# Kernel tuning notes

Hardware: AMD Instinct MI355X
Metric: run time of the kernel (lower is better)

Reference implementation:

```python
import jax, jax.numpy as jnp
import numpy as np

L, M, K, H, F, D = 8, 32768, 8, 128, 32, 3  # fronts, nodes/front, in-degree, hidden, feat, depth-branches


def _resnet(x, w1, b1, w2, b2, w3, b3):
    # resnet module: lay3(tanh(lay2(tanh(lay1(x)))) + x)
    h1 = jnp.tanh(x @ w1 + b1)
    h2 = jnp.tanh(h1 @ w2 + b2)
    return (h2 + x) @ w3 + b3


def setup_inputs() -> dict:
    key = jax.random.key(0)
    ks = iter(jax.random.split(key, 80))

    def nrm(shape, fan_in):
        return jax.random.normal(next(ks), shape, jnp.float32) / np.float32(np.sqrt(fan_in))

    def bias(shape):
        return 0.01 * jax.random.normal(next(ks), shape, jnp.float32)

    inp = {}
    inp["node_feats"] = jax.random.normal(next(ks), (L, M, F), jnp.float32)
    inp["pred_idx"] = jax.random.randint(next(ks), (L - 1, M, K), 0, M, jnp.int32)
    inp["embed_w"] = nrm((F, H), F); inp["embed_b"] = bias((H,))
    # d{1,2,3}_mp_bwd and d{1,2,3}_mp_bwd1 : per-depth pair of H-resnets, stacked [D,2,...]
    inp["mp_w1"] = nrm((D, 2, H, H), H); inp["mp_b1"] = bias((D, 2, H))
    inp["mp_w2"] = nrm((D, 2, H, H), H); inp["mp_b2"] = bias((D, 2, H))
    inp["mp_w3"] = nrm((D, 2, H, H), H); inp["mp_b3"] = bias((D, 2, H))
    for p in ("comb", "node"):  # d*_comb_embed(+1), d*_node_embeds(+1)
        inp[p + "_wide_w1"] = nrm((D, 2 * H, 2 * H), 2 * H); inp[p + "_wide_b1"] = bias((D, 2 * H))
        inp[p + "_wide_w2"] = nrm((D, 2 * H, 2 * H), 2 * H); inp[p + "_wide_b2"] = bias((D, 2 * H))
        inp[p + "_wide_w3"] = nrm((D, 2 * H, H), 2 * H);     inp[p + "_wide_b3"] = bias((D, H))
        inp[p + "_h_w1"] = nrm((D, H, H), H); inp[p + "_h_b1"] = bias((D, H))
        inp[p + "_h_w2"] = nrm((D, H, H), H); inp[p + "_h_b2"] = bias((D, H))
        inp[p + "_h_w3"] = nrm((D, H, H), H); inp[p + "_h_b3"] = bias((D, H))
    return inp


def reference(node_feats, pred_idx, embed_w, embed_b,
              mp_w1, mp_b1, mp_w2, mp_b2, mp_w3, mp_b3,
              comb_wide_w1, comb_wide_b1, comb_wide_w2, comb_wide_b2, comb_wide_w3, comb_wide_b3,
              comb_h_w1, comb_h_b1, comb_h_w2, comb_h_b2, comb_h_w3, comb_h_b3,
              node_wide_w1, node_wide_b1, node_wide_w2, node_wide_b2, node_wide_w3, node_wide_b3,
              node_h_w1, node_h_b1, node_h_w2, node_h_b2, node_h_w3, node_h_b3):
    # front 0 (topological roots): apply_func only -> tanh(embed_op(feats))
    e = jnp.tanh(node_feats[0] @ embed_w + embed_b)          # [M, H]
    outs = [e]
    prev = e
    for l in range(1, L):
        d = min(l - 1, 2)                                    # bwd_depth branch (d1/d2/d3)
        # msg_func + redux_func: gather mailbox from predecessor front, sum-reduce, MLP
        s = prev[pred_idx[l - 1]].sum(axis=1)                # [M, K, H] -> [M, H]
        r = jnp.tanh(_resnet(s, mp_w1[d, 0], mp_b1[d, 0], mp_w2[d, 0], mp_b2[d, 0], mp_w3[d, 0], mp_b3[d, 0]))
        r = jnp.tanh(_resnet(r, mp_w1[d, 1], mp_b1[d, 1], mp_w2[d, 1], mp_b2[d, 1], mp_w3[d, 1], mp_b3[d, 1]))
        # apply_func: embed, comb branch (bwd_node_embeds is all-zero for not-yet-processed nodes),
        # then node_embeds branch on cat(embeds, msgs_redux)
        e = jnp.tanh(node_feats[l] @ embed_w + embed_b)
        c = jnp.concatenate([e, jnp.zeros_like(e)], axis=-1)  # [M, 2H]
        e = jnp.tanh(_resnet(c, comb_wide_w1[d], comb_wide_b1[d], comb_wide_w2[d], comb_wide_b2[d], comb_wide_w3[d], comb_wide_b3[d]))
        e = jnp.tanh(_resnet(e, comb_h_w1[d], comb_h_b1[d], comb_h_w2[d], comb_h_b2[d], comb_h_w3[d], comb_h_b3[d]))
        c2 = jnp.concatenate([e, r], axis=-1)                 # [M, 2H]
        e = jnp.tanh(_resnet(c2, node_wide_w1[d], node_wide_b1[d], node_wide_w2[d], node_wide_b2[d], node_wide_w3[d], node_wide_b3[d]))
        e = jnp.tanh(_resnet(e, node_h_w1[d], node_h_b1[d], node_h_w2[d], node_h_b2[d], node_h_w3[d], node_h_b3[d]))
        outs.append(e)
        prev = e
    return jnp.stack(outs)                                    # graph.ndata['bwd_node_embeds'] : [L, M, H]
```

## Files before the change

### kernel.cpp

```cpp
#include <hip/hip_runtime.h>
#include <hip/hip_bf16.h>

#define M_NODES 32768

using f16x8 = __attribute__((ext_vector_type(8))) _Float16;
using f32x4 = __attribute__((ext_vector_type(4))) float;
typedef unsigned short u16;
typedef unsigned int   u32;

__device__ __forceinline__ u16 f2h(float f){
  _Float16 h = (_Float16)f;
  return __builtin_bit_cast(u16, h);
}
__device__ __forceinline__ float h2f(u16 h){
  return (float)__builtin_bit_cast(_Float16, h);
}
__device__ __forceinline__ float tanh_fast(float x){
  float t = __builtin_amdgcn_exp2f(x * 2.8853900817779268f);
  return 1.0f - 2.0f * __builtin_amdgcn_rcpf(t + 1.0f);
}

struct PrepPtrs { const float* p[16]; };

__global__ void prep_kernel(PrepPtrs pp, u16* ws){
  const int Bc[16] = {1,6,6,6,3,3,3,3,3,3,3,3,3,3,3,3};
  const int Kc[16] = {32,128,128,128,256,256,256,128,128,128,256,256,256,128,128,128};
  const int Nc[16] = {128,128,128,128,256,256,128,128,128,128,256,256,128,128,128,128};
  const int tot = 1576960;
  for (int i = blockIdx.x*blockDim.x + threadIdx.x; i < tot; i += gridDim.x*blockDim.x){
    int e = i, s = 0;
    while (true){ int sz = Bc[s]*Kc[s]*Nc[s]; if (e < sz) break; e -= sz; ++s; }
    int K = Kc[s], N = Nc[s];
    int kn = K*N;
    int b = e / kn; int r2 = e - b*kn;
    int n = r2 / K; int k = r2 - n*K;
    float v = pp.p[s][(size_t)b*kn + (size_t)k*N + n];
    ws[i] = f2h(v);
  }
}

__global__ __launch_bounds__(256) void front0_kernel(const float* __restrict__ feats,
                                                     const float* __restrict__ ew,
                                                     const float* __restrict__ eb,
                                                     float* __restrict__ out){
  __shared__ float fl[2048];
  const int brow = blockIdx.x * 64;
  const float* f0 = feats + (size_t)brow*32;
#pragma unroll
  for (int it = 0; it < 2; ++it){
    int idx = threadIdx.x + it*256;
    *(float4*)(&fl[idx*4]) = *(const float4*)(f0 + idx*4);
  }
  __syncthreads();
  const int col = threadIdx.x & 127, rh = threadIdx.x >> 7;
  float w[32];
#pragma unroll
  for (int k = 0; k < 32; ++k) w[k] = ew[k*128 + col];
  const float bv = eb[col];
  for (int r = 0; r < 32; ++r){
    int row = rh*32 + r;
    float acc = bv;
#pragma unroll
    for (int k = 0; k < 32; ++k) acc += fl[row*32 + k] * w[k];
    out[(size_t)(brow + row)*128 + col] = tanh_fast(acc);
  }
}

template<int KLOOP, int N, int WS, int AMODE, int RESMODE, int OUTMODE, bool INPLACE>
__device__ __forceinline__ void mm_stage(const u16* inA, u16* outB, const u16* resB,
                                         const u16* __restrict__ wt,
                                         const float* __restrict__ bias,
                                         float* gout)
{
  const int tid  = threadIdx.x;
  const int lane = tid & 63, nq = tid >> 6;
  const int q = lane >> 4, c = lane & 15;
  constexpr int NT = N / 64;
  constexpr int NP = KLOOP / 32;
  const float* inAf = (const float*)inA;
  float*       outF = (float*)outB;
  const float* resF = (const float*)resB;

  const u16* wrow[NT];
#pragma unroll
  for (int j = 0; j < NT; ++j){
    int nt = nq*2 + (j & 1) + (j >> 1) * 8;
    wrow[j] = wt + (size_t)(nt*16 + c)*WS + q*8;
  }
  f16x8 breg[2][NT];
#pragma unroll
  for (int j = 0; j < NT; ++j) breg[0][j] = *(const f16x8*)(wrow[j]);
#pragma unroll
  for (int j = 0; j < NT; ++j) breg[1][j] = *(const f16x8*)(wrow[j] + 32);

  f32x4 acc[4][NT];
#pragma unroll
  for (int m = 0; m < 4; ++m)
#pragma unroll
    for (int j = 0; j < NT; ++j) acc[m][j] = (f32x4){0.f,0.f,0.f,0.f};

#pragma unroll
  for (int kp = 0; kp < NP; ++kp){
    f16x8 bc[NT];
#pragma unroll
    for (int j = 0; j < NT; ++j) bc[j] = breg[kp & 1][j];
    if (kp + 2 < NP){
#pragma unroll
      for (int j = 0; j < NT; ++j) breg[kp & 1][j] = *(const f16x8*)(wrow[j] + (kp + 2)*32);
    }
#pragma unroll
    for (int m = 0; m < 4; ++m){
      if (AMODE == 0){
        f16x8 af = *(const f16x8*)(&inA[(m*16 + c)*264 + kp*32 + q*8]);
#pragma unroll
        for (int j = 0; j < NT; ++j)
          acc[m][j] = __builtin_amdgcn_mfma_f32_16x16x32_f16(af, bc[j], acc[m][j], 0, 0, 0);
      } else {
        const float* ap = inAf + (m*16 + c)*132 + kp*32 + q*8;
        float4 x0 = *(const float4*)(ap);
        float4 x1 = *(const float4*)(ap + 4);
        float xs[8] = {x0.x,x0.y,x0.z,x0.w,x1.x,x1.y,x1.z,x1.w};
        f16x8 ah, al;
#pragma unroll
        for (int k = 0; k < 8; ++k){
          _Float16 hi = (_Float16)xs[k];
          ah[k] = hi;
          al[k] = (_Float16)(xs[k] - (float)hi);
        }
#pragma unroll
        for (int j = 0; j < NT; ++j){
          acc[m][j] = __builtin_amdgcn_mfma_f32_16x16x32_f16(ah, bc[j], acc[m][j], 0, 0, 0);
          acc[m][j] = __builtin_amdgcn_mfma_f32_16x16x32_f16(al, bc[j], acc[m][j], 0, 0, 0);
        }
      }
    }
  }
  if (INPLACE) __syncthreads();
#pragma unroll
  for (int j = 0; j < NT; ++j){
    int nt = nq*2 + (j & 1) + (j >> 1) * 8;
    int col = nt*16 + c;
    float bv = bias[col];
#pragma unroll
    for (int m = 0; m < 4; ++m){
#pragma unroll
      for (int r = 0; r < 4; ++r){
        int row = m*16 + q*4 + r;
        float v = tanh_fast(acc[m][j][r] + bv);
        if (RESMODE == 2)      v += h2f(resB[row*264 + col]);
        else if (RESMODE == 1){ if (col < 128) v += h2f(resB[row*264 + col]); }
        else if (RESMODE == 3) v += resF[row*132 + col];
        if (OUTMODE == 2)      gout[(size_t)row*128 + col] = v;
        else if (OUTMODE == 1) outF[row*132 + col] = v;
        else                   outB[row*264 + col] = f2h(v);
      }
    }
  }
  __syncthreads();
}

__device__ __forceinline__ void embed_stage(const float* __restrict__ featsRow,
                                            u16* outB, const u16* __restrict__ wt,
                                            const float* __restrict__ bias)
{
  const int tid  = threadIdx.x;
  const int lane = tid & 63, nq = tid >> 6;
  const int q = lane >> 4, c = lane & 15;
  f16x8 bf[2];
#pragma unroll
  for (int j = 0; j < 2; ++j){
    int nt = nq*2 + j;
    bf[j] = *(const f16x8*)(wt + (nt*16 + c)*32 + q*8);
  }
  f32x4 acc[4][2];
#pragma unroll
  for (int m = 0; m < 4; ++m){ acc[m][0] = (f32x4){0,0,0,0}; acc[m][1] = (f32x4){0,0,0,0}; }
#pragma unroll
  for (int m = 0; m < 4; ++m){
    int row = m*16 + c;
    const float* fp = featsRow + (size_t)row*32 + q*8;
    float4 a0 = *(const float4*)(fp);
    float4 a1 = *(const float4*)(fp + 4);
    float xs[8] = {a0.x,a0.y,a0.z,a0.w,a1.x,a1.y,a1.z,a1.w};
    f16x8 ah, al;
#pragma unroll
    for (int k = 0; k < 8; ++k){
      _Float16 hi = (_Float16)xs[k];
      ah[k] = hi;
      al[k] = (_Float16)(xs[k] - (float)hi);
    }
#pragma unroll
    for (int j = 0; j < 2; ++j){
      acc[m][j] = __builtin_amdgcn_mfma_f32_16x16x32_f16(ah, bf[j], acc[m][j], 0, 0, 0);
      acc[m][j] = __builtin_amdgcn_mfma_f32_16x16x32_f16(al, bf[j], acc[m][j], 0, 0, 0);
    }
  }
#pragma unroll
  for (int j = 0; j < 2; ++j){
    int nt = nq*2 + j;
    int col = nt*16 + c;
    float bv = bias[col];
#pragma unroll
    for (int m = 0; m < 4; ++m){
#pragma unroll
      for (int r = 0; r < 4; ++r){
        int row = m*16 + q*4 + r;
        outB[row*264 + col] = f2h(tanh_fast(acc[m][j][r] + bv));
      }
    }
  }
  __syncthreads();
}

struct FrontArgs {
  const float* feats; const int* pred;
  const u16* ws;
  float* out;
  const float* embed_b;
  const float* mp_b1; const float* mp_b2; const float* mp_b3;
  const float* cw_b1; const float* cw_b2; const float* cw_b3;
  const float* ch_b1; const float* ch_b2; const float* ch_b3;
  const float* nw_b1; const float* nw_b2; const float* nw_b3;
  const float* nh_b1; const float* nh_b2; const float* nh_b3;
  int l, d;
};

__global__ __launch_bounds__(256, 2) void front_kernel(FrontArgs A)
{
  extern __shared__ u16 lds[];
  u16* P  = lds;
  u16* Q  = lds + 16896;
  const int brow = blockIdx.x * 64;
  const int d = A.d;
  const u16* ws = A.ws;

  {
    float* Pf = (float*)P;
    const float* prev = A.out + (size_t)(A.l - 1) * M_NODES * 128;
    const int c4 = threadIdx.x & 31;
    const int r0 = threadIdx.x >> 5;
#pragma unroll
    for (int rr = 0; rr < 8; ++rr){
      int row = r0 + rr*8;
      const int* ip = A.pred + ((size_t)(A.l - 1) * M_NODES + brow + row) * 8;
      float sx=0.f, sy=0.f, sz=0.f, sw=0.f;
#pragma unroll
      for (int p = 0; p < 8; ++p){
        const float4 v = *(const float4*)(prev + (size_t)ip[p]*128 + c4*4);
        sx += v.x; sy += v.y; sz += v.z; sw += v.w;
      }
      float4 o = {sx, sy, sz, sw};
      *(float4*)(&Pf[row*132 + c4*4]) = o;
    }
  }
  __syncthreads();

  const int d0 = d*2, d1 = d*2 + 1;
  mm_stage<128,128,128, 1,0,0,false>(P, Q, nullptr, ws + 4096   + (size_t)d0*16384, A.mp_b1 + d0*128, nullptr);
  mm_stage<128,128,128, 0,3,1,false>(Q, P, P,       ws + 102400 + (size_t)d0*16384, A.mp_b2 + d0*128, nullptr);
  mm_stage<128,128,128, 1,0,0,false>(P, Q, nullptr, ws + 200704 + (size_t)d0*16384, A.mp_b3 + d0*128, nullptr);
  mm_stage<128,128,128, 0,0,0,false>(Q, P, nullptr, ws + 4096   + (size_t)d1*16384, A.mp_b1 + d1*128, nullptr);
  mm_stage<128,128,128, 0,2,1,true >(P, P, Q,       ws + 102400 + (size_t)d1*16384, A.mp_b2 + d1*128, nullptr);
  mm_stage<128,128,128, 1,0,0,false>(P, Q + 128, nullptr, ws + 200704 + (size_t)d1*16384, A.mp_b3 + d1*128, nullptr);
  embed_stage(A.feats + ((size_t)A.l * M_NODES + brow) * 32, Q, ws, A.embed_b);
  mm_stage<128,256,256, 0,0,0,false>(Q, P, nullptr, ws + 299008 + (size_t)d*65536, A.cw_b1 + d*256, nullptr);
  mm_stage<256,256,256, 0,1,0,true >(P, P, Q,       ws + 495616 + (size_t)d*65536, A.cw_b2 + d*256, nullptr);
  mm_stage<256,128,256, 0,0,0,false>(P, Q, nullptr, ws + 692224 + (size_t)d*32768, A.cw_b3 + d*128, nullptr);
  mm_stage<128,128,128, 0,0,0,false>(Q, P, nullptr, ws + 790528 + (size_t)d*16384, A.ch_b1 + d*128, nullptr);
  mm_stage<128,128,128, 0,2,0,true >(P, P, Q,       ws + 839680 + (size_t)d*16384, A.ch_b2 + d*128, nullptr);
  mm_stage<128,128,128, 0,0,0,false>(P, Q, nullptr, ws + 888832 + (size_t)d*16384, A.ch_b3 + d*128, nullptr);
  mm_stage<256,256,256, 0,0,0,false>(Q, P, nullptr, ws + 937984  + (size_t)d*65536, A.nw_b1 + d*256, nullptr);
  mm_stage<256,256,256, 0,2,0,true >(P, P, Q,       ws + 1134592 + (size_t)d*65536, A.nw_b2 + d*256, nullptr);
  mm_stage<256,128,256, 0,0,0,false>(P, Q, nullptr, ws + 1331200 + (size_t)d*32768, A.nw_b3 + d*128, nullptr);
  mm_stage<128,128,128, 0,0,0,false>(Q, P, nullptr, ws + 1429504 + (size_t)d*16384, A.nh_b1 + d*128, nullptr);
  mm_stage<128,128,128, 0,2,0,true >(P, P, Q,       ws + 1478656 + (size_t)d*16384, A.nh_b2 + d*128, nullptr);
  float* gout = A.out + ((size_t)A.l * M_NODES + brow) * 128;
  mm_stage<128,128,128, 0,0,2,false>(P, nullptr, nullptr, ws + 1527808 + (size_t)d*16384, A.nh_b3 + d*128, gout);
}

extern "C" void kernel_launch(void* const* d_in, const int* in_sizes, int n_in,
                              void* d_out, int out_size, void* d_ws, size_t ws_size,
                              hipStream_t stream)
{
  (void)in_sizes; (void)n_in; (void)out_size; (void)ws_size;
  const float* feats = (const float*)d_in[0];
  const int*   pred  = (const int*)d_in[1];
  u16*   ws  = (u16*)d_ws;
  float* out = (float*)d_out;

  PrepPtrs pp;
  const int wIdx[16] = {2,4,6,8,10,12,14,16,18,20,22,24,26,28,30,32};
  for (int i = 0; i < 16; ++i) pp.p[i] = (const float*)d_in[wIdx[i]];
  prep_kernel<<<2048, 256, 0, stream>>>(pp, ws);

  front0_kernel<<<M_NODES/64, 256, 0, stream>>>(feats, (const float*)d_in[2], (const float*)d_in[3], out);

  const size_t LDSB = (size_t)(2*64*264) * sizeof(u16);
  (void)hipFuncSetAttribute((const void*)front_kernel,
                            hipFuncAttributeMaxDynamicSharedMemorySize, (int)LDSB);

  FrontArgs A;
  A.feats = feats; A.pred = pred; A.ws = ws; A.out = out;
  A.embed_b = (const float*)d_in[3];
  A.mp_b1 = (const float*)d_in[5];  A.mp_b2 = (const float*)d_in[7];  A.mp_b3 = (const float*)d_in[9];
  A.cw_b1 = (const float*)d_in[11]; A.cw_b2 = (const float*)d_in[13]; A.cw_b3 = (const float*)d_in[15];
  A.ch_b1 = (const float*)d_in[17]; A.ch_b2 = (const float*)d_in[19]; A.ch_b3 = (const float*)d_in[21];
  A.nw_b1 = (const float*)d_in[23]; A.nw_b2 = (const float*)d_in[25]; A.nw_b3 = (const float*)d_in[27];
  A.nh_b1 = (const float*)d_in[29]; A.nh_b2 = (const float*)d_in[31]; A.nh_b3 = (const float*)d_in[33];

  for (int l = 1; l < 8; ++l){
    A.l = l;
    A.d = (l - 1 < 2) ? (l - 1) : 2;
    front_kernel<<<M_NODES/64, 256, LDSB, stream>>>(A);
  }
}
```

Measured before the change: 700.6 us.

## Drive front kernel stages from a runtime table with rotated K-panel order

Replaces the fully inlined sequence of templated matmul stages with a runtime loop over a 19-entry stage descriptor table passed in kernel args, calling two NT-specialised non-inlined stage bodies. The aim is to shrink code size and instruction-cache pressure, and to let each block start its K-panel loop at an offset based on block index so that concurrent blocks read different weight rows and spread the load traffic. Biases are gathered once into a contiguous workspace region by the prep kernel. In exchange the stage parameters become runtime branches, and the K loop is no longer unrolled, which may cost scheduling quality and add overhead from the masked indexing and rolled loop.

```diff
diff --git a/kernel.cpp b/kernel.cpp
--- a/kernel.cpp
+++ b/kernel.cpp
@@ -20,7 +20,9 @@
   return 1.0f - 2.0f * __builtin_amdgcn_rcpf(t + 1.0f);
 }
 
-struct PrepPtrs { const float* p[16]; };
+struct PrepPtrs { const float* w[16]; const float* b[16]; };
+
+#define BIAS_BASE 1576960
 
 __global__ void prep_kernel(PrepPtrs pp, u16* ws){
   const int Bc[16] = {1,6,6,6,3,3,3,3,3,3,3,3,3,3,3,3};
@@ -34,8 +36,15 @@
     int kn = K*N;
     int b = e / kn; int r2 = e - b*kn;
     int n = r2 / K; int k = r2 - n*K;
-    float v = pp.p[s][(size_t)b*kn + (size_t)k*N + n];
-    ws[i] = f2h(v);
+    ws[i] = f2h(pp.w[s][(size_t)b*kn + (size_t)k*N + n]);
+  }
+  float* bb = (float*)(ws + BIAS_BASE);
+  const int bs[16] = {128,768,768,768,768,768,384,384,384,384,768,768,384,384,384,384};
+  const int btot = 8576;
+  for (int i = blockIdx.x*blockDim.x + threadIdx.x; i < btot; i += gridDim.x*blockDim.x){
+    int e = i, s = 0;
+    while (e >= bs[s]){ e -= bs[s]; ++s; }
+    bb[i] = pp.b[s][e];
   }
 }
 
@@ -66,80 +75,105 @@
   }
 }
 
-template<int KLOOP, int N, int WS, int AMODE, int RESMODE, int OUTMODE, bool INPLACE>
-__device__ __forceinline__ void mm_stage(const u16* inA, u16* outB, const u16* resB,
-                                         const u16* __restrict__ wt,
-                                         const float* __restrict__ bias,
-                                         float* gout)
+struct StageRec { int wt; int bias; u32 fl; };
+
+template<int NT>
+__device__ __forceinline__ void compute_panel(f32x4 (&acc)[4][NT], f16x8 (&bc)[NT],
+                                              const u16* inA, const float* inAf,
+                                              int kpp, int amode, int q, int c)
+{
+  if (amode == 0){
+#pragma unroll
+    for (int m = 0; m < 4; ++m){
+      f16x8 af = *(const f16x8*)(&inA[(m*16 + c)*264 + kpp*32 + q*8]);
+#pragma unroll
+      for (int j = 0; j < NT; ++j)
+        acc[m][j] = __builtin_amdgcn_mfma_f32_16x16x32_f16(af, bc[j], acc[m][j], 0, 0, 0);
+    }
+  } else {
+#pragma unroll
+    for (int m = 0; m < 4; ++m){
+      const float* ap = inAf + (m*16 + c)*132 + kpp*32 + q*8;
+      float4 x0 = *(const float4*)(ap);
+      float4 x1 = *(const float4*)(ap + 4);
+      float xs[8] = {x0.x,x0.y,x0.z,x0.w,x1.x,x1.y,x1.z,x1.w};
+      f16x8 ah, al;
+#pragma unroll
+      for (int k = 0; k < 8; ++k){
+        _Float16 hi = (_Float16)xs[k];
+        ah[k] = hi;
+        al[k] = (_Float16)(xs[k] - (float)hi);
+      }
+#pragma unroll
+      for (int j = 0; j < NT; ++j)
+        acc[m][j] = __builtin_amdgcn_mfma_f32_16x16x32_f16(ah, bc[j], acc[m][j], 0, 0, 0);
+#pragma unroll
+      for (int j = 0; j < NT; ++j)
+        acc[m][j] = __builtin_amdgcn_mfma_f32_16x16x32_f16(al, bc[j], acc[m][j], 0, 0, 0);
+    }
+  }
+}
+
+template<int NT>
+__device__ void stage_body(const u16* inA, u16* outB, const u16* resB,
+                           const u16* __restrict__ wt, int wstride,
+                           const float* __restrict__ bias, float* gout,
+                           int NP, int amode, int res, int outm, int inplace, int ph)
 {
   const int tid  = threadIdx.x;
   const int lane = tid & 63, nq = tid >> 6;
   const int q = lane >> 4, c = lane & 15;
-  constexpr int NT = N / 64;
-  constexpr int NP = KLOOP / 32;
   const float* inAf = (const float*)inA;
   float*       outF = (float*)outB;
   const float* resF = (const float*)resB;
+  const int msk = NP - 1;
 
   const u16* wrow[NT];
 #pragma unroll
   for (int j = 0; j < NT; ++j){
-    int nt = nq*2 + (j & 1) + (j >> 1) * 8;
-    wrow[j] = wt + (size_t)(nt*16 + c)*WS + q*8;
-  }
-  f16x8 breg[2][NT];
-#pragma unroll
-  for (int j = 0; j < NT; ++j) breg[0][j] = *(const f16x8*)(wrow[j]);
-#pragma unroll
-  for (int j = 0; j < NT; ++j) breg[1][j] = *(const f16x8*)(wrow[j] + 32);
-
+    int nt_ = nq*2 + (j & 1) + (j >> 1) * 8;
+    wrow[j] = wt + (size_t)(nt_*16 + c)*wstride + q*8;
+  }
+  f16x8 br0[NT], br1[NT];
+  {
+    int p0 = ph & msk, p1 = (ph + 1) & msk;
+#pragma unroll
+    for (int j = 0; j < NT; ++j) br0[j] = *(const f16x8*)(wrow[j] + p0*32);
+#pragma unroll
+    for (int j = 0; j < NT; ++j) br1[j] = *(const f16x8*)(wrow[j] + p1*32);
+  }
   f32x4 acc[4][NT];
 #pragma unroll
   for (int m = 0; m < 4; ++m)
 #pragma unroll
     for (int j = 0; j < NT; ++j) acc[m][j] = (f32x4){0.f,0.f,0.f,0.f};
 
-#pragma unroll
-  for (int kp = 0; kp < NP; ++kp){
-    f16x8 bc[NT];
-#pragma unroll
-    for (int j = 0; j < NT; ++j) bc[j] = breg[kp & 1][j];
-    if (kp + 2 < NP){
-#pragma unroll
-      for (int j = 0; j < NT; ++j) breg[kp & 1][j] = *(const f16x8*)(wrow[j] + (kp + 2)*32);
-    }
-#pragma unroll
-    for (int m = 0; m < 4; ++m){
-      if (AMODE == 0){
-        f16x8 af = *(const f16x8*)(&inA[(m*16 + c)*264 + kp*32 + q*8]);
-#pragma unroll
-        for (int j = 0; j < NT; ++j)
-          acc[m][j] = __builtin_amdgcn_mfma_f32_16x16x32_f16(af, bc[j], acc[m][j], 0, 0, 0);
-      } else {
-        const float* ap = inAf + (m*16 + c)*132 + kp*32 + q*8;
-        float4 x0 = *(const float4*)(ap);
-        float4 x1 = *(const float4*)(ap + 4);
-        float xs[8] = {x0.x,x0.y,x0.z,x0.w,x1.x,x1.y,x1.z,x1.w};
-        f16x8 ah, al;
-#pragma unroll
-        for (int k = 0; k < 8; ++k){
-          _Float16 hi = (_Float16)xs[k];
-          ah[k] = hi;
-          al[k] = (_Float16)(xs[k] - (float)hi);
-        }
-#pragma unroll
-        for (int j = 0; j < NT; ++j){
-          acc[m][j] = __builtin_amdgcn_mfma_f32_16x16x32_f16(ah, bc[j], acc[m][j], 0, 0, 0);
-          acc[m][j] = __builtin_amdgcn_mfma_f32_16x16x32_f16(al, bc[j], acc[m][j], 0, 0, 0);
-        }
-      }
-    }
-  }
-  if (INPLACE) __syncthreads();
+#pragma clang loop unroll(disable)
+  for (int kp = 0; kp < NP; kp += 2){
+    {
+      int kpp = (ph + kp) & msk;
+      compute_panel<NT>(acc, br0, inA, inAf, kpp, amode, q, c);
+      if (kp + 2 < NP){
+        int kn = (ph + kp + 2) & msk;
+#pragma unroll
+        for (int j = 0; j < NT; ++j) br0[j] = *(const f16x8*)(wrow[j] + kn*32);
+      }
+    }
+    {
+      int kpp = (ph + kp + 1) & msk;
+      compute_panel<NT>(acc, br1, inA, inAf, kpp, amode, q, c);
+      if (kp + 3 < NP){
+        int kn = (ph + kp + 3) & msk;
+#pragma unroll
+        for (int j = 0; j < NT; ++j) br1[j] = *(const f16x8*)(wrow[j] + kn*32);
+      }
+    }
+  }
+  if (inplace) __syncthreads();
 #pragma unroll
   for (int j = 0; j < NT; ++j){
-    int nt = nq*2 + (j & 1) + (j >> 1) * 8;
-    int col = nt*16 + c;
+    int nt_ = nq*2 + (j & 1) + (j >> 1) * 8;
+    int col = nt_*16 + c;
     float bv = bias[col];
 #pragma unroll
     for (int m = 0; m < 4; ++m){
@@ -147,21 +181,21 @@
       for (int r = 0; r < 4; ++r){
         int row = m*16 + q*4 + r;
         float v = tanh_fast(acc[m][j][r] + bv);
-        if (RESMODE == 2)      v += h2f(resB[row*264 + col]);
-        else if (RESMODE == 1){ if (col < 128) v += h2f(resB[row*264 + col]); }
-        else if (RESMODE == 3) v += resF[row*132 + col];
-        if (OUTMODE == 2)      gout[(size_t)row*128 + col] = v;
-        else if (OUTMODE == 1) outF[row*132 + col] = v;
-        else                   outB[row*264 + col] = f2h(v);
+        if (res == 2)      v += h2f(resB[row*264 + col]);
+        else if (res == 1){ if (col < 128) v += h2f(resB[row*264 + col]); }
+        else if (res == 3) v += resF[row*132 + col];
+        if (outm == 2)      gout[(size_t)row*128 + col] = v;
+        else if (outm == 1) outF[row*132 + col] = v;
+        else                outB[row*264 + col] = f2h(v);
       }
     }
   }
   __syncthreads();
 }
 
-__device__ __forceinline__ void embed_stage(const float* __restrict__ featsRow,
-                                            u16* outB, const u16* __restrict__ wt,
-                                            const float* __restrict__ bias)
+__device__ void embed_stage(const float* __restrict__ featsRow,
+                            u16* outB, const u16* __restrict__ wt,
+                            const float* __restrict__ bias)
 {
   const int tid  = threadIdx.x;
   const int lane = tid & 63, nq = tid >> 6;
@@ -169,8 +203,8 @@
   f16x8 bf[2];
 #pragma unroll
   for (int j = 0; j < 2; ++j){
-    int nt = nq*2 + j;
-    bf[j] = *(const f16x8*)(wt + (nt*16 + c)*32 + q*8);
+    int nt_ = nq*2 + j;
+    bf[j] = *(const f16x8*)(wt + (nt_*16 + c)*32 + q*8);
   }
   f32x4 acc[4][2];
 #pragma unroll
@@ -197,8 +231,8 @@
   }
 #pragma unroll
   for (int j = 0; j < 2; ++j){
-    int nt = nq*2 + j;
-    int col = nt*16 + c;
+    int nt_ = nq*2 + j;
+    int col = nt_*16 + c;
     float bv = bias[col];
 #pragma unroll
     for (int m = 0; m < 4; ++m){
@@ -216,26 +250,20 @@
   const float* feats; const int* pred;
   const u16* ws;
   float* out;
-  const float* embed_b;
-  const float* mp_b1; const float* mp_b2; const float* mp_b3;
-  const float* cw_b1; const float* cw_b2; const float* cw_b3;
-  const float* ch_b1; const float* ch_b2; const float* ch_b3;
-  const float* nw_b1; const float* nw_b2; const float* nw_b3;
-  const float* nh_b1; const float* nh_b2; const float* nh_b3;
-  int l, d;
+  int l;
+  StageRec st[19];
 };
 
 __global__ __launch_bounds__(256, 2) void front_kernel(FrontArgs A)
 {
   extern __shared__ u16 lds[];
-  u16* P  = lds;
-  u16* Q  = lds + 16896;
+  u16* B0 = lds;
+  u16* B1 = lds + 16896;
   const int brow = blockIdx.x * 64;
-  const int d = A.d;
-  const u16* ws = A.ws;
+  const int ph = blockIdx.x;
 
   {
-    float* Pf = (float*)P;
+    float* Pf = (float*)B0;
     const float* prev = A.out + (size_t)(A.l - 1) * M_NODES * 128;
     const int c4 = threadIdx.x & 31;
     const int r0 = threadIdx.x >> 5;
@@ -255,27 +283,38 @@
   }
   __syncthreads();
 
-  const int d0 = d*2, d1 = d*2 + 1;
-  mm_stage<128,128,128, 1,0,0,false>(P, Q, nullptr, ws + 4096   + (size_t)d0*16384, A.mp_b1 + d0*128, nullptr);
-  mm_stage<128,128,128, 0,3,1,false>(Q, P, P,       ws + 102400 + (size_t)d0*16384, A.mp_b2 + d0*128, nullptr);
-  mm_stage<128,128,128, 1,0,0,false>(P, Q, nullptr, ws + 200704 + (size_t)d0*16384, A.mp_b3 + d0*128, nullptr);
-  mm_stage<128,128,128, 0,0,0,false>(Q, P, nullptr, ws + 4096   + (size_t)d1*16384, A.mp_b1 + d1*128, nullptr);
-  mm_stage<128,128,128, 0,2,1,true >(P, P, Q,       ws + 102400 + (size_t)d1*16384, A.mp_b2 + d1*128, nullptr);
-  mm_stage<128,128,128, 1,0,0,false>(P, Q + 128, nullptr, ws + 200704 + (size_t)d1*16384, A.mp_b3 + d1*128, nullptr);
-  embed_stage(A.feats + ((size_t)A.l * M_NODES + brow) * 32, Q, ws, A.embed_b);
-  mm_stage<128,256,256, 0,0,0,false>(Q, P, nullptr, ws + 299008 + (size_t)d*65536, A.cw_b1 + d*256, nullptr);
-  mm_stage<256,256,256, 0,1,0,true >(P, P, Q,       ws + 495616 + (size_t)d*65536, A.cw_b2 + d*256, nullptr);
-  mm_stage<256,128,256, 0,0,0,false>(P, Q, nullptr, ws + 692224 + (size_t)d*32768, A.cw_b3 + d*128, nullptr);
-  mm_stage<128,128,128, 0,0,0,false>(Q, P, nullptr, ws + 790528 + (size_t)d*16384, A.ch_b1 + d*128, nullptr);
-  mm_stage<128,128,128, 0,2,0,true >(P, P, Q,       ws + 839680 + (size_t)d*16384, A.ch_b2 + d*128, nullptr);
-  mm_stage<128,128,128, 0,0,0,false>(P, Q, nullptr, ws + 888832 + (size_t)d*16384, A.ch_b3 + d*128, nullptr);
-  mm_stage<256,256,256, 0,0,0,false>(Q, P, nullptr, ws + 937984  + (size_t)d*65536, A.nw_b1 + d*256, nullptr);
-  mm_stage<256,256,256, 0,2,0,true >(P, P, Q,       ws + 1134592 + (size_t)d*65536, A.nw_b2 + d*256, nullptr);
-  mm_stage<256,128,256, 0,0,0,false>(P, Q, nullptr, ws + 1331200 + (size_t)d*32768, A.nw_b3 + d*128, nullptr);
-  mm_stage<128,128,128, 0,0,0,false>(Q, P, nullptr, ws + 1429504 + (size_t)d*16384, A.nh_b1 + d*128, nullptr);
-  mm_stage<128,128,128, 0,2,0,true >(P, P, Q,       ws + 1478656 + (size_t)d*16384, A.nh_b2 + d*128, nullptr);
+  const float* biasb = (const float*)(A.ws + BIAS_BASE);
   float* gout = A.out + ((size_t)A.l * M_NODES + brow) * 128;
-  mm_stage<128,128,128, 0,0,2,false>(P, nullptr, nullptr, ws + 1527808 + (size_t)d*16384, A.nh_b3 + d*128, gout);
+
+#pragma clang loop unroll(disable)
+  for (int s = 0; s < 19; ++s){
+    const int wt_off = A.st[s].wt;
+    const int b_off  = A.st[s].bias;
+    const u32 fl     = A.st[s].fl;
+    if (fl & (1u << 17)){
+      embed_stage(A.feats + ((size_t)A.l * M_NODES + brow) * 32, B1, A.ws, biasb);
+      continue;
+    }
+    const int NP      = fl & 15;
+    const int wstride = (fl & (1u << 4)) ? 256 : 128;
+    const int amode   = (fl >> 6) & 1;
+    const int res     = (fl >> 8) & 3;
+    const int outm    = (fl >> 10) & 3;
+    const int ip      = (fl >> 12) & 1;
+    const u16* inA = (fl & (1u << 13)) ? B1 : B0;
+    const int ob = (fl >> 14) & 3;
+    u16* outB = (ob == 0) ? B0 : ((ob == 1) ? B1 : (B1 + 128));
+    const u16* resB = (fl & (1u << 16)) ? B1 : B0;
+    if (fl & (1u << 5))
+      stage_body<4>(inA, outB, resB, A.ws + wt_off, wstride, biasb + b_off, gout, NP, amode, res, outm, ip, ph);
+    else
+      stage_body<2>(inA, outB, resB, A.ws + wt_off, wstride, biasb + b_off, gout, NP, amode, res, outm, ip, ph);
+  }
+}
+
+static inline u32 mkfl(int np,int ws256,int nt4,int am,int res,int outm,int ip,int inb,int outb,int resb,int emb){
+  return (u32)np | (u32)(ws256<<4) | (u32)(nt4<<5) | (u32)(am<<6) | (u32)(res<<8) | (u32)(outm<<10)
+       | (u32)(ip<<12) | (u32)(inb<<13) | (u32)(outb<<14) | (u32)(resb<<16) | (u32)(emb<<17);
 }
 
 extern "C" void kernel_launch(void* const* d_in, const int* in_sizes, int n_in,
@@ -290,7 +329,8 @@
 
   PrepPtrs pp;
   const int wIdx[16] = {2,4,6,8,10,12,14,16,18,20,22,24,26,28,30,32};
-  for (int i = 0; i < 16; ++i) pp.p[i] = (const float*)d_in[wIdx[i]];
+  const int bIdx[16] = {3,5,7,9,11,13,15,17,19,21,23,25,27,29,31,33};
+  for (int i = 0; i < 16; ++i){ pp.w[i] = (const float*)d_in[wIdx[i]]; pp.b[i] = (const float*)d_in[bIdx[i]]; }
   prep_kernel<<<2048, 256, 0, stream>>>(pp, ws);
 
   front0_kernel<<<M_NODES/64, 256, 0, stream>>>(feats, (const float*)d_in[2], (const float*)d_in[3], out);
@@ -301,16 +341,31 @@
 
   FrontArgs A;
   A.feats = feats; A.pred = pred; A.ws = ws; A.out = out;
-  A.embed_b = (const float*)d_in[3];
-  A.mp_b1 = (const float*)d_in[5];  A.mp_b2 = (const float*)d_in[7];  A.mp_b3 = (const float*)d_in[9];
-  A.cw_b1 = (const float*)d_in[11]; A.cw_b2 = (const float*)d_in[13]; A.cw_b3 = (const float*)d_in[15];
-  A.ch_b1 = (const float*)d_in[17]; A.ch_b2 = (const float*)d_in[19]; A.ch_b3 = (const float*)d_in[21];
-  A.nw_b1 = (const float*)d_in[23]; A.nw_b2 = (const float*)d_in[25]; A.nw_b3 = (const float*)d_in[27];
-  A.nh_b1 = (const float*)d_in[29]; A.nh_b2 = (const float*)d_in[31]; A.nh_b3 = (const float*)d_in[33];
 
   for (int l = 1; l < 8; ++l){
     A.l = l;
-    A.d = (l - 1 < 2) ? (l - 1) : 2;
+    const int d = (l - 1 < 2) ? (l - 1) : 2;
+    const int d0 = d*2, d1 = d*2 + 1;
+    StageRec* S = A.st;
+    S[0]  = {4096    + d0*16384, 128  + d0*128, mkfl(4,0,0, 1,0,0, 0, 0,1,0, 0)};
+    S[1]  = {102400  + d0*16384, 896  + d0*128, mkfl(4,0,0, 0,3,1, 0, 1,0,0, 0)};
+    S[2]  = {200704  + d0*16384, 1664 + d0*128, mkfl(4,0,0, 1,0,0, 0, 0,1,0, 0)};
+    S[3]  = {4096    + d1*16384, 128  + d1*128, mkfl(4,0,0, 0,0,0, 0, 1,0,0, 0)};
+    S[4]  = {102400  + d1*16384, 896  + d1*128, mkfl(4,0,0, 0,2,1, 1, 0,0,1, 0)};
+    S[5]  = {200704  + d1*16384, 1664 + d1*128, mkfl(4,0,0, 1,0,0, 0, 0,2,0, 0)};
+    S[6]  = {0, 0,                               mkfl(0,0,0, 0,0,0, 0, 0,1,0, 1)};
+    S[7]  = {299008  + d*65536,  2432 + d*256,  mkfl(4,1,1, 0,0,0, 0, 1,0,0, 0)};
+    S[8]  = {495616  + d*65536,  3200 + d*256,  mkfl(8,1,1, 0,1,0, 1, 0,0,1, 0)};
+    S[9]  = {692224  + d*32768,  3968 + d*128,  mkfl(8,1,0, 0,0,0, 0, 0,1,0, 0)};
+    S[10] = {790528  + d*16384,  4352 + d*128,  mkfl(4,0,0, 0,0,0, 0, 1,0,0, 0)};
+    S[11] = {839680  + d*16384,  4736 + d*128,  mkfl(4,0,0, 0,2,0, 1, 0,0,1, 0)};
+    S[12] = {888832  + d*16384,  5120 + d*128,  mkfl(4,0,0, 0,0,0, 0, 0,1,0, 0)};
+    S[13] = {937984  + d*65536,  5504 + d*256,  mkfl(8,1,1, 0,0,0, 0, 1,0,0, 0)};
+    S[14] = {1134592 + d*65536,  6272 + d*256,  mkfl(8,1,1, 0,2,0, 1, 0,0,1, 0)};
+    S[15] = {1331200 + d*32768,  7040 + d*128,  mkfl(8,1,0, 0,0,0, 0, 0,1,0, 0)};
+    S[16] = {1429504 + d*16384,  7424 + d*128,  mkfl(4,0,0, 0,0,0, 0, 1,0,0, 0)};
+    S[17] = {1478656 + d*16384,  7808 + d*128,  mkfl(4,0,0, 0,2,0, 1, 0,0,1, 0)};
+    S[18] = {1527808 + d*16384,  8192 + d*128,  mkfl(4,0,0, 0,0,2, 0, 0,0,0, 0)};
     front_kernel<<<M_NODES/64, 256, LDSB, stream>>>(A);
   }
 }
```

Result: slower. 1.286 ms (+83.5%).
